# Optimization experiments

Hardware: AMD Instinct MI355X
Metric: run time of the kernel (lower is better)

## Reference

```python
import jax, jax.numpy as jnp
import numpy as np

K = 3
KK = K * K
EPS = 1e-5


def conv2d(x, w, b, pad):
    y = jax.lax.conv_general_dilated(x, w, (1, 1), [(pad, pad), (pad, pad)],
                                     dimension_numbers=("NCHW", "OIHW", "NCHW"))
    return y + b[None, :, None, None]


def bn(x, g, b, m, v):
    inv = g / jnp.sqrt(v + EPS)
    return x * inv[None, :, None, None] + (b - m * inv)[None, :, None, None]


def deform_sample(x, dy, dx):
    # x: [B,C,H,W]; dy,dx: [B,KK,H,W] -> sampled [B,C,KK,H,W] (bilinear, zeros outside)
    B, C, H, W = x.shape
    k = jnp.arange(K, dtype=x.dtype) - 1.0  # pad=1, dilation=1, stride=1
    ky = jnp.repeat(k, K)  # [KK] row offsets
    kx = jnp.tile(k, K)    # [KK] col offsets
    hh = jnp.arange(H, dtype=x.dtype)
    ww = jnp.arange(W, dtype=x.dtype)
    py = hh[None, :, None] + ky[:, None, None] + dy  # [B,KK,H,W]
    px = ww[None, None, :] + kx[:, None, None] + dx

    def sample_one(img, py, px):
        y0f = jnp.floor(py); x0f = jnp.floor(px)
        wy = py - y0f; wx = px - x0f
        y0 = y0f.astype(jnp.int32); x0 = x0f.astype(jnp.int32)

        def gather(yi, xi, w):
            valid = (yi >= 0) & (yi < H) & (xi >= 0) & (xi < W)
            yc = jnp.clip(yi, 0, H - 1); xc = jnp.clip(xi, 0, W - 1)
            v = img[:, yc, xc]  # [C,KK,H,W]
            return v * (w * valid)[None]

        return (gather(y0, x0, (1 - wy) * (1 - wx)) +
                gather(y0, x0 + 1, (1 - wy) * wx) +
                gather(y0 + 1, x0, wy * (1 - wx)) +
                gather(y0 + 1, x0 + 1, wy * wx))

    return jax.vmap(sample_one)(x, py, px)


def setup_inputs() -> dict:
    key = jax.random.key(0)
    ks = jax.random.split(key, 16)
    B, C, H, W = 8, 256, 64, 64
    d = {
        "feature": jax.random.normal(ks[0], (B, C, H, W), jnp.float32),
        "p1_w": jax.random.normal(ks[1], (C, C, 1, 1), jnp.float32) * 0.05,
        "p1_b": jax.random.normal(ks[2], (C,), jnp.float32) * 0.05,
        "bn1_g": jax.random.normal(ks[3], (C,), jnp.float32) * 0.1 + 1.0,
        "bn1_b": jax.random.normal(ks[4], (C,), jnp.float32) * 0.05,
        "bn1_m": jax.random.normal(ks[5], (C,), jnp.float32) * 0.05,
        "bn1_v": jax.random.uniform(ks[6], (C,), jnp.float32) + 0.5,
        "off_w": jax.random.normal(ks[7], (3 * KK, 2 * C, K, K), jnp.float32) * 0.01,
        "off_b": jax.random.normal(ks[8], (3 * KK,), jnp.float32) * 0.01,
        "dcn_w": jax.random.normal(ks[9], (C, C, K, K), jnp.float32) * 0.05,
        "dcn_b": jax.random.normal(ks[10], (C,), jnp.float32) * 0.05,
        "bn2_g": jax.random.normal(ks[11], (C,), jnp.float32) * 0.1 + 1.0,
        "bn2_b": jax.random.normal(ks[12], (C,), jnp.float32) * 0.05,
        "bn2_m": jax.random.normal(ks[13], (C,), jnp.float32) * 0.05,
        "bn2_v": jax.random.uniform(ks[14], (C,), jnp.float32) + 0.5,
    }
    return d


def reference(feature, p1_w, p1_b, bn1_g, bn1_b, bn1_m, bn1_v,
              off_w, off_b, dcn_w, dcn_b, bn2_g, bn2_b, bn2_m, bn2_v):
    flipped = feature[..., ::-1]                      # flip last (W) axis
    proj = bn(conv2d(feature, p1_w, p1_b, 0), bn1_g, bn1_b, bn1_m, bn1_v)
    # DCNv2: offsets/mask from concat(flipped, proj)
    concat = jnp.concatenate([flipped, proj], axis=1)
    off = conv2d(concat, off_w, off_b, 1)             # [B,27,H,W]
    dy = off[:, :KK]
    dx = off[:, KK:2 * KK]
    mask = jax.nn.sigmoid(off[:, 2 * KK:])            # [B,KK,H,W]
    sampled = deform_sample(flipped, dy, dx)          # [B,C,KK,H,W]
    O = dcn_w.shape[0]
    y = jnp.einsum("bckhw,ock->bohw", sampled * mask[:, None], dcn_w.reshape(O, -1, KK))
    y = y + dcn_b[None, :, None, None]
    y = bn(y, bn2_g, bn2_b, bn2_m, bn2_v)
    return jax.nn.relu(proj + y)
```

## Files before the change

kernel.cpp:

```cpp
#include <hip/hip_runtime.h>
#include <hip/hip_bf16.h>
#include <math.h>

typedef __attribute__((ext_vector_type(8))) short short8;
typedef __attribute__((ext_vector_type(4))) short short4v;
typedef __attribute__((ext_vector_type(4))) float f32x4;
typedef __attribute__((ext_vector_type(2))) float f32x2;

__device__ __forceinline__ float bs2f(short s){
    union { unsigned u; float f; } x; x.u = ((unsigned)(unsigned short)s) << 16; return x.f;
}
__device__ __forceinline__ short f2bs(float f){
    union { float f; unsigned u; } x; x.f = f;
    unsigned r = x.u + 0x7fff + ((x.u >> 16) & 1);
    return (short)(r >> 16);
}
__device__ __forceinline__ f32x2 up2(unsigned u){
    union { unsigned u; float f; } lo, hi;
    lo.u = u << 16; hi.u = u & 0xffff0000u;
    f32x2 r; r.x = lo.f; r.y = hi.f; return r;
}
__device__ __forceinline__ unsigned pk2rn(float lo, float hi){
    __hip_bfloat162 h = __float22bfloat162_rn(make_float2(lo, hi));
    union { __hip_bfloat162 h; unsigned u; } cv; cv.h = h; return cv.u;
}
__device__ __forceinline__ void gl2lds16(const void* g, void* l){
    __builtin_amdgcn_global_load_lds(
        (const __attribute__((address_space(1))) void*)g,
        (__attribute__((address_space(3))) void*)l, 16, 0, 0);
}
__device__ __forceinline__ void hard_barrier(){
    __builtin_amdgcn_sched_barrier(0);
    __builtin_amdgcn_s_barrier();
    __builtin_amdgcn_sched_barrier(0);
}

#define XPB ((size_t)66*66*512)


__global__ void k_prep(const float* __restrict__ p1_w, const float* __restrict__ p1_b,
                       const float* __restrict__ bn1_g, const float* __restrict__ bn1_b,
                       const float* __restrict__ bn1_m, const float* __restrict__ bn1_v,
                       const float* __restrict__ off_w,
                       const float* __restrict__ dcn_w, const float* __restrict__ dcn_b,
                       const float* __restrict__ bn2_g, const float* __restrict__ bn2_b,
                       const float* __restrict__ bn2_m, const float* __restrict__ bn2_v,
                       short* __restrict__ p1_wb, short* __restrict__ Woffb,
                       short* __restrict__ Wbf,
                       float* __restrict__ bias1f, float* __restrict__ inv2f,
                       float* __restrict__ bias2f, unsigned* __restrict__ XpadU)
{
    int blk = blockIdx.x, t = threadIdx.x;
    if (blk == 0) {
        float inv1 = bn1_g[t] / sqrtf(bn1_v[t] + 1e-5f);
        bias1f[t] = p1_b[t] * inv1 + bn1_b[t] - bn1_m[t] * inv1;
        float inv2 = bn2_g[t] / sqrtf(bn2_v[t] + 1e-5f);
        inv2f[t] = inv2;
        bias2f[t] = dcn_b[t] * inv2 + bn2_b[t] - bn2_m[t] * inv2;
    } else if (blk <= 256) {
        int o = blk - 1;
        float inv1 = bn1_g[o] / sqrtf(bn1_v[o] + 1e-5f);
        p1_wb[o*256 + t] = f2bs(p1_w[o*256 + t] * inv1);
    } else if (blk <= 512) {
        int o = blk - 257;
        const float* src = dcn_w + (size_t)o*2304;
        #pragma unroll
        for (int j = 0; j < 9; ++j)
            Wbf[(size_t)o*2304 + j*256 + t] = f2bs(src[t*9 + j]);
    } else if (blk <= 544) {
        int oc = blk - 513;
        if (oc < 27) {
            const float* src = off_w + (size_t)oc*4608;
            #pragma unroll
            for (int j = 0; j < 18; ++j) {
                int e = j*256 + t, tap = e >> 9, ci = e & 511;
                Woffb[(size_t)oc*4608 + e] = f2bs(src[ci*9 + tap]);
            }
        } else {
            #pragma unroll
            for (int j = 0; j < 18; ++j)
                Woffb[(size_t)oc*4608 + j*256 + t] = 0;
        }
    } else {
        int hb = blk - 545;
        int b = hb / 260, i = hb % 260;
        int y, x;
        if (i < 66)       { y = 0;  x = i; }
        else if (i < 132) { y = 65; x = i - 66; }
        else { int j = i - 132; y = 1 + (j >> 1); x = (j & 1) * 65; }
        XpadU[((size_t)(b*66 + y)*66 + x)*256 + t] = 0u;
    }
}

__global__ void k_featT(const float* __restrict__ feature, short* __restrict__ Xpad)
{
    __shared__ float tile[64][65];
    int bb = blockIdx.x;
    int b = bb & 7, h = (bb >> 3) & 63, cg = bb >> 9;
    int c0 = cg * 64;
    int t = threadIdx.x;
    int lw = t & 63, li = t >> 6;
    #pragma unroll
    for (int j = 0; j < 16; ++j) {
        int cl = j*4 + li;
        tile[cl][63 - lw] = feature[((b*256 + c0 + cl)*64 + h)*64 + lw];
    }
    __syncthreads();
    #pragma unroll
    for (int j = 0; j < 16; ++j) {
        int wl = j*4 + li;
        Xpad[((size_t)(b*66 + h+1)*66 + (wl+1))*512 + c0 + lw] = f2bs(tile[lw][wl]);
    }
}

__global__ __launch_bounds__(512, 4) void k_projm(
    short* Xpad, const short* __restrict__ p1_wb, const float* __restrict__ bias1f)
{
    __shared__ short Ash[256*32];
    __shared__ short Bsh[64*32];
    int bid = blockIdx.x;
    int b = bid & 7, h = bid >> 3;
    int t = threadIdx.x;
    int lane = t & 63, w = t >> 6;
    int ln = lane & 15, q = lane >> 4;
    int r16 = lane >> 2;
    int sq  = (lane & 3) ^ ((lane >> 3) & 3);
    int rq  = (q ^ ((ln >> 1) & 3)) * 8;
    size_t rowbase = (size_t)(b*66 + h + 1)*66;

    f32x4 acc[2][4] = {};
    for (int kt = 0; kt < 8; ++kt) {
        int kcol = kt*32 + sq*8;
        #pragma unroll
        for (int i = 0; i < 2; ++i) {
            int row = w*32 + i*16 + r16;
            gl2lds16(p1_wb + (size_t)row*256 + kcol, Ash + (w*32 + i*16)*32);
        }
        if (w < 4) {
            int x = w*16 + r16;
            gl2lds16(Xpad + (rowbase + (64 - x))*512 + kcol, Bsh + (w*16)*32);
        }
        __syncthreads();
        short8 af[2], bfr[4];
        #pragma unroll
        for (int i = 0; i < 2; ++i)
            af[i] = *(const short8*)&Ash[(w*32 + i*16 + ln)*32 + rq];
        #pragma unroll
        for (int j = 0; j < 4; ++j)
            bfr[j] = *(const short8*)&Bsh[(j*16 + ln)*32 + rq];
        #pragma unroll
        for (int i = 0; i < 2; ++i)
            #pragma unroll
            for (int j = 0; j < 4; ++j)
                acc[i][j] = __builtin_amdgcn_mfma_f32_16x16x32_bf16(af[i], bfr[j], acc[i][j], 0, 0, 0);
        __syncthreads();
    }
    #pragma unroll
    for (int i = 0; i < 2; ++i) {
        int ob = w*32 + i*16 + q*4;
        #pragma unroll
        for (int j = 0; j < 4; ++j) {
            int x = j*16 + ln;
            size_t xb = (rowbase + x + 1)*512 + 256 + ob;
            short4v st;
            st.x = f2bs(acc[i][j][0] + bias1f[ob]);
            st.y = f2bs(acc[i][j][1] + bias1f[ob+1]);
            st.z = f2bs(acc[i][j][2] + bias1f[ob+2]);
            st.w = f2bs(acc[i][j][3] + bias1f[ob+3]);
            *(short4v*)&Xpad[xb] = st;
        }
    }
}

__global__ __launch_bounds__(512, 4) void k_offm(
    const short* __restrict__ Xpad, const short* __restrict__ Woffb,
    const float* __restrict__ off_b, float* __restrict__ offv)
{
    __shared__ short Ash[8][32*32];
    __shared__ short Bsh[8][64*32];
    int bid = blockIdx.x;
    int b = bid & 7, h = bid >> 3;
    int t = threadIdx.x;
    int lane = t & 63, w = t >> 6;
    int ln = lane & 15, q = lane >> 4;
    int wr = w >> 2, wc = w & 3;
    int r16 = lane >> 2;
    int sq  = (lane & 3) ^ ((lane >> 3) & 3);
    int rq  = (q ^ ((ln >> 1) & 3)) * 8;
    const short* xb = Xpad + (size_t)b*XPB;

    f32x4 acc = {};
    for (int it = 0; it < 18; ++it) {
        #pragma unroll
        for (int s = 0; s < 8; ++s) {
            int k = it*256 + s*32;
            int tap = k >> 9;
            int dy = tap/3 - 1, dx = tap%3 - 1;
            if (w < 4) {
                int row = w*16 + r16;
                const short* gB = xb + ((size_t)(h + 1 + dy)*66 + (row + dx + 1))*512
                                     + (k & 511) + sq*8;
                gl2lds16(gB, &Bsh[s][(w*16)*32]);
            } else if (w < 6) {
                int row = (w-4)*16 + r16;
                const short* gA = Woffb + (size_t)row*4608 + k + sq*8;
                gl2lds16(gA, &Ash[s][((w-4)*16)*32]);
            }
        }
        __syncthreads();
        #pragma unroll
        for (int s = 0; s < 8; ++s) {
            short8 af  = *(const short8*)&Ash[s][(wr*16 + ln)*32 + rq];
            short8 bfr = *(const short8*)&Bsh[s][(wc*16 + ln)*32 + rq];
            acc = __builtin_amdgcn_mfma_f32_16x16x32_bf16(af, bfr, acc, 0, 0, 0);
        }
        __syncthreads();
    }
    int x = wc*16 + ln;
    #pragma unroll
    for (int r = 0; r < 4; ++r) {
        int oc = wr*16 + q*4 + r;
        if (oc < 27)
            offv[((b*27 + oc)*64 + h)*64 + x] = acc[r] + off_b[oc];
    }
}

__global__ __launch_bounds__(512, 4) void k_gemm(
    const short* __restrict__ Xpad,
    const short* __restrict__ Wbf,
    const float* __restrict__ offv,
    const float* __restrict__ inv2f, const float* __restrict__ bias2f,
    float* __restrict__ out)
{
    __shared__ __align__(16) short Ash[2][256*32];
    __shared__ __align__(16) short Bsh[2][64*32];
    __shared__ unsigned c_pk[576];
    __shared__ float c_w[576*4];
    int bid = blockIdx.x;
    int b = bid & 7, h = bid >> 3;
    int t = threadIdx.x;
    int lane = t & 63, w = t >> 6;
    int ln = lane & 15, q = lane >> 4;
    int r16 = lane >> 2;
    int sq  = (lane & 3) ^ ((lane >> 3) & 3);
    int rq  = (q ^ ((ln >> 1) & 3)) * 8;

    for (int e = t; e < 576; e += 512) {
        int p = e / 9, k = e % 9;
        int base = (b*27)*4096 + h*64 + p;
        float dy = offv[base + k*4096];
        float dx = offv[base + (9+k)*4096];
        float ms = offv[base + (18+k)*4096];
        ms = 1.f / (1.f + expf(-ms));
        float py = (float)h + (float)(k/3 - 1) + dy;
        float px = (float)p + (float)(k%3 - 1) + dx;
        float y0f = floorf(py), x0f = floorf(px);
        float wy = py - y0f, wx = px - x0f;
        int y0 = (int)y0f, x0 = (int)x0f;
        int y1 = y0 + 1, x1 = x0 + 1;
        float vy0 = (y0 >= 0 && y0 < 64) ? 1.f : 0.f;
        float vy1 = (y1 >= 0 && y1 < 64) ? 1.f : 0.f;
        float vx0 = (x0 >= 0 && x0 < 64) ? 1.f : 0.f;
        float vx1 = (x1 >= 0 && x1 < 64) ? 1.f : 0.f;
        int y0c = min(max(y0,0),63), y1c = min(max(y1,0),63);
        int x0c = min(max(x0,0),63), x1c = min(max(x1,0),63);
        unsigned cell = (unsigned)(((y0c+1)*66 + x0c+1)*128);
        unsigned sx = (x1c != x0c) ? 1u : 0u;
        unsigned sy = (y1c != y0c) ? 1u : 0u;
        c_pk[e] = cell | (sx << 20) | (sy << 21);
        c_w[e*4+0] = ms * (1.f-wy)*(1.f-wx) * vy0*vx0;
        c_w[e*4+1] = ms * (1.f-wy)*wx       * vy0*vx1;
        c_w[e*4+2] = ms * wy*(1.f-wx)       * vy1*vx0;
        c_w[e*4+3] = ms * wy*wx             * vy1*vx1;
    }
    __syncthreads();

    const uint2* fT = (const uint2*)Xpad + (size_t)b*(XPB/4);
    int pr = t >> 3;
    int jo = t & 7;
    int pe9 = pr*9;
    short* bdst = &Bsh[jo >> 2][pr*32 + (((jo & 3) ^ ((pr >> 1) & 3)) << 3)];

    f32x4 acc[2][4] = {};
    uint4 U[4], V[4];

    auto GATHER = [&](int win, uint4 (&dst)[4]) {
        unsigned pw = c_pk[pe9 + (win >> 2)];
        int o00 = pw & 0xFFFFF;
        int dxs = (pw >> 13) & 128;
        int dys = ((pw >> 8) & 0x2000) | ((pw >> 13) & 0x100);
        int cin = ((win & 3) << 4) + jo*2;
        const uint2* p0 = fT + (o00 + cin);
        dst[0] = *(const uint4*)(p0);
        dst[1] = *(const uint4*)(p0 + dxs);
        dst[2] = *(const uint4*)(p0 + dys);
        dst[3] = *(const uint4*)(p0 + dys + dxs);
    };

    auto WIN = [&](int kc2, uint4 (&uc)[4], uint4 (&vn)[4]) {
        int tap = kc2 >> 2;
        #pragma unroll
        for (int s = 0; s < 2; ++s) {
            int kcol = (kc2*2 + s)*32 + sq*8;
            #pragma unroll
            for (int i = 0; i < 2; ++i) {
                int row = w*32 + i*16 + r16;
                gl2lds16(Wbf + (size_t)row*2304 + kcol, &Ash[s][(w*32 + i*16)*32]);
            }
        }
        __builtin_amdgcn_sched_barrier(0);
        GATHER(kc2 < 35 ? kc2 + 1 : 35, vn);
        const float4 cw = *(const float4*)&c_w[(pe9 + tap)*4];
        f32x2 Wx; Wx.x = cw.x; Wx.y = cw.x;
        f32x2 Wy; Wy.x = cw.y; Wy.y = cw.y;
        f32x2 Wz; Wz.x = cw.z; Wz.y = cw.z;
        f32x2 Ww; Ww.x = cw.w; Ww.y = cw.w;
        f32x2 G0 = Wx*up2(uc[0].x) + Wy*up2(uc[1].x) + Wz*up2(uc[2].x) + Ww*up2(uc[3].x);
        f32x2 G1 = Wx*up2(uc[0].y) + Wy*up2(uc[1].y) + Wz*up2(uc[2].y) + Ww*up2(uc[3].y);
        f32x2 G2 = Wx*up2(uc[0].z) + Wy*up2(uc[1].z) + Wz*up2(uc[2].z) + Ww*up2(uc[3].z);
        f32x2 G3 = Wx*up2(uc[0].w) + Wy*up2(uc[1].w) + Wz*up2(uc[2].w) + Ww*up2(uc[3].w);
        uint4 pkv;
        pkv.x = pk2rn(G0.x, G0.y);
        pkv.y = pk2rn(G1.x, G1.y);
        pkv.z = pk2rn(G2.x, G2.y);
        pkv.w = pk2rn(G3.x, G3.y);
        *(uint4*)bdst = pkv;
        asm volatile("s_waitcnt vmcnt(4) lgkmcnt(0)" ::: "memory");
        hard_barrier();
        #pragma unroll
        for (int s = 0; s < 2; ++s) {
            short8 af[2], bfr[4];
            #pragma unroll
            for (int i = 0; i < 2; ++i)
                af[i] = *(const short8*)&Ash[s][(w*32 + i*16 + ln)*32 + rq];
            #pragma unroll
            for (int jj = 0; jj < 4; ++jj)
                bfr[jj] = *(const short8*)&Bsh[s][(jj*16 + ln)*32 + rq];
            #pragma unroll
            for (int i = 0; i < 2; ++i)
                #pragma unroll
                for (int jj = 0; jj < 4; ++jj)
                    acc[i][jj] = __builtin_amdgcn_mfma_f32_16x16x32_bf16(af[i], bfr[jj], acc[i][jj], 0, 0, 0);
        }
        hard_barrier();
    };

    GATHER(0, U);
    __builtin_amdgcn_sched_barrier(0);
    for (int kc2 = 0; kc2 < 36; kc2 += 2) {
        WIN(kc2, U, V);
        WIN(kc2 + 1, V, U);
    }

    #pragma unroll
    for (int i = 0; i < 2; ++i) {
        int ob = w*32 + i*16 + q*4;
        #pragma unroll
        for (int jj = 0; jj < 4; ++jj) {
            int p = jj*16 + ln;
            size_t xb = ((size_t)(b*66 + h + 1)*66 + p + 1)*512 + 256 + ob;
            short4v prr = *(const short4v*)&Xpad[xb];
            #pragma unroll
            for (int r = 0; r < 4; ++r) {
                int o = ob + r;
                size_t idx = ((size_t)(b*256 + o))*4096 + h*64 + p;
                float rs = bs2f(((const short*)&prr)[r]);
                float v = rs + acc[i][jj][r]*inv2f[o] + bias2f[o];
                out[idx] = v < 0.f ? 0.f : v;
            }
        }
    }
}

extern "C" void kernel_launch(void* const* d_in, const int* in_sizes, int n_in,
                              void* d_out, int out_size, void* d_ws, size_t ws_size,
                              hipStream_t stream)
{
    const float* feature = (const float*)d_in[0];
    const float* p1_w  = (const float*)d_in[1];
    const float* p1_b  = (const float*)d_in[2];
    const float* bn1_g = (const float*)d_in[3];
    const float* bn1_b = (const float*)d_in[4];
    const float* bn1_m = (const float*)d_in[5];
    const float* bn1_v = (const float*)d_in[6];
    const float* off_w = (const float*)d_in[7];
    const float* off_b = (const float*)d_in[8];
    const float* dcn_w = (const float*)d_in[9];
    const float* dcn_b = (const float*)d_in[10];
    const float* bn2_g = (const float*)d_in[11];
    const float* bn2_b = (const float*)d_in[12];
    const float* bn2_m = (const float*)d_in[13];
    const float* bn2_v = (const float*)d_in[14];

    float* ws = (float*)d_ws;
    short* Xpad   = (short*)ws;
    float* offbuf = ws + 8921088;
    short* p1_wb  = (short*)(ws + 9805824);
    short* Woffb  = (short*)(ws + 9838592);
    short* Wbf    = (short*)(ws + 9912320);
    float* bias1f = ws + 10207232;
    float* inv2f  = ws + 10207488;
    float* bias2f = ws + 10207744;

    k_prep<<<2625, 256, 0, stream>>>(p1_w, p1_b, bn1_g, bn1_b, bn1_m, bn1_v,
                                     off_w, dcn_w, dcn_b, bn2_g, bn2_b, bn2_m, bn2_v,
                                     p1_wb, Woffb, Wbf, bias1f, inv2f, bias2f,
                                     (unsigned*)Xpad);
    k_featT<<<2048, 256, 0, stream>>>(feature, Xpad);
    k_projm<<<512, 512, 0, stream>>>(Xpad, p1_wb, bias1f);
    k_offm<<<512, 512, 0, stream>>>(Xpad, Woffb, off_b, offbuf);
    k_gemm<<<512, 512, 0, stream>>>(Xpad, Wbf, offbuf, inv2f, bias2f, (float*)d_out);
}
```

Baseline: 218.9 us.

## Replace direct global-to-LDS loads with register-prefetched double buffering in GEMM kernels

Both the projection GEMM and the deformable-conv GEMM stop using global_load_lds for weight/activation tiles. They now load the next tile into registers one step ahead and write the current tile to LDS just before the barrier. The aim is to hide global load latency behind the MFMA work of the previous step, instead of waiting on vmcnt before each barrier. In exchange the kernels use more VGPRs, which can lower occupancy, and they spend extra instructions on the register-to-LDS store.

After: 392.5 us. +79.3%, slower.

```diff
diff --git a/kernel.cpp b/kernel.cpp
--- a/kernel.cpp
+++ b/kernel.cpp
@@ -31,6 +31,12 @@
 }
 __device__ __forceinline__ void hard_barrier(){
     __builtin_amdgcn_sched_barrier(0);
+    __builtin_amdgcn_s_barrier();
+    __builtin_amdgcn_sched_barrier(0);
+}
+__device__ __forceinline__ void lds_barrier(){
+    __builtin_amdgcn_sched_barrier(0);
+    asm volatile("s_waitcnt lgkmcnt(0)" ::: "memory");
     __builtin_amdgcn_s_barrier();
     __builtin_amdgcn_sched_barrier(0);
 }
@@ -116,8 +122,8 @@
 __global__ __launch_bounds__(512, 4) void k_projm(
     short* Xpad, const short* __restrict__ p1_wb, const float* __restrict__ bias1f)
 {
-    __shared__ short Ash[256*32];
-    __shared__ short Bsh[64*32];
+    __shared__ __align__(16) short Ash[256*32];
+    __shared__ __align__(16) short Bsh[64*32];
     int bid = blockIdx.x;
     int b = bid & 7, h = bid >> 3;
     int t = threadIdx.x;
@@ -129,18 +135,26 @@
     size_t rowbase = (size_t)(b*66 + h + 1)*66;
 
     f32x4 acc[2][4] = {};
-    for (int kt = 0; kt < 8; ++kt) {
+    uint4 a0[2], a1[2], b0, b1;
+
+    auto LOADR = [&](int kt, uint4 (&ar)[2], uint4& br){
         int kcol = kt*32 + sq*8;
         #pragma unroll
-        for (int i = 0; i < 2; ++i) {
-            int row = w*32 + i*16 + r16;
-            gl2lds16(p1_wb + (size_t)row*256 + kcol, Ash + (w*32 + i*16)*32);
-        }
+        for (int i = 0; i < 2; ++i)
+            ar[i] = *(const uint4*)(p1_wb + (size_t)(w*32 + i*16 + r16)*256 + kcol);
         if (w < 4) {
             int x = w*16 + r16;
-            gl2lds16(Xpad + (rowbase + (64 - x))*512 + kcol, Bsh + (w*16)*32);
-        }
-        __syncthreads();
+            br = *(const uint4*)(Xpad + (rowbase + (64 - x))*512 + kcol);
+        }
+    };
+    auto WRITE = [&](uint4 (&ar)[2], uint4& br){
+        #pragma unroll
+        for (int i = 0; i < 2; ++i)
+            *(uint4*)&Ash[(w*32 + i*16)*32 + lane*8] = ar[i];
+        if (w < 4)
+            *(uint4*)&Bsh[(w*16)*32 + lane*8] = br;
+    };
+    auto MM = [&](){
         short8 af[2], bfr[4];
         #pragma unroll
         for (int i = 0; i < 2; ++i)
@@ -153,7 +167,24 @@
             #pragma unroll
             for (int j = 0; j < 4; ++j)
                 acc[i][j] = __builtin_amdgcn_mfma_f32_16x16x32_bf16(af[i], bfr[j], acc[i][j], 0, 0, 0);
-        __syncthreads();
+    };
+
+    LOADR(0, a0, b0);
+    __builtin_amdgcn_sched_barrier(0);
+    #pragma unroll 1
+    for (int kt = 0; kt < 8; kt += 2) {
+        LOADR(kt + 1, a1, b1);
+        __builtin_amdgcn_sched_barrier(0);
+        WRITE(a0, b0);
+        lds_barrier();
+        MM();
+        hard_barrier();
+        LOADR(kt < 6 ? kt + 2 : 7, a0, b0);
+        __builtin_amdgcn_sched_barrier(0);
+        WRITE(a1, b1);
+        lds_barrier();
+        MM();
+        hard_barrier();
     }
     #pragma unroll
     for (int i = 0; i < 2; ++i) {
@@ -283,6 +314,7 @@
 
     f32x4 acc[2][4] = {};
     uint4 U[4], V[4];
+    uint4 A0[4], A1[4];
 
     auto GATHER = [&](int win, uint4 (&dst)[4]) {
         unsigned pw = c_pk[pe9 + (win >> 2)];
@@ -296,20 +328,22 @@
         dst[2] = *(const uint4*)(p0 + dys);
         dst[3] = *(const uint4*)(p0 + dys + dxs);
     };
-
-    auto WIN = [&](int kc2, uint4 (&uc)[4], uint4 (&vn)[4]) {
+    auto ALOADR = [&](int kc2, uint4 (&ar)[4]) {
+        #pragma unroll
+        for (int s = 0; s < 2; ++s)
+            #pragma unroll
+            for (int i = 0; i < 2; ++i)
+                ar[s*2+i] = *(const uint4*)(Wbf
+                    + (size_t)(w*32 + i*16 + r16)*2304 + (kc2*2 + s)*32 + sq*8);
+    };
+
+    auto WIN = [&](int kc2, uint4 (&arC)[4], uint4 (&arN)[4],
+                   uint4 (&uc)[4], uint4 (&vn)[4]) {
+        int kn = kc2 < 35 ? kc2 + 1 : 35;
+        ALOADR(kn, arN);
+        GATHER(kn, vn);
+        __builtin_amdgcn_sched_barrier(0);
         int tap = kc2 >> 2;
-        #pragma unroll
-        for (int s = 0; s < 2; ++s) {
-            int kcol = (kc2*2 + s)*32 + sq*8;
-            #pragma unroll
-            for (int i = 0; i < 2; ++i) {
-                int row = w*32 + i*16 + r16;
-                gl2lds16(Wbf + (size_t)row*2304 + kcol, &Ash[s][(w*32 + i*16)*32]);
-            }
-        }
-        __builtin_amdgcn_sched_barrier(0);
-        GATHER(kc2 < 35 ? kc2 + 1 : 35, vn);
         const float4 cw = *(const float4*)&c_w[(pe9 + tap)*4];
         f32x2 Wx; Wx.x = cw.x; Wx.y = cw.x;
         f32x2 Wy; Wy.x = cw.y; Wy.y = cw.y;
@@ -325,8 +359,12 @@
         pkv.z = pk2rn(G2.x, G2.y);
         pkv.w = pk2rn(G3.x, G3.y);
         *(uint4*)bdst = pkv;
-        asm volatile("s_waitcnt vmcnt(4) lgkmcnt(0)" ::: "memory");
-        hard_barrier();
+        #pragma unroll
+        for (int s = 0; s < 2; ++s)
+            #pragma unroll
+            for (int i = 0; i < 2; ++i)
+                *(uint4*)&Ash[s][(w*32 + i*16)*32 + lane*8] = arC[s*2+i];
+        lds_barrier();
         #pragma unroll
         for (int s = 0; s < 2; ++s) {
             short8 af[2], bfr[4];
@@ -345,11 +383,12 @@
         hard_barrier();
     };
 
+    ALOADR(0, A0);
     GATHER(0, U);
     __builtin_amdgcn_sched_barrier(0);
     for (int kc2 = 0; kc2 < 36; kc2 += 2) {
-        WIN(kc2, U, V);
-        WIN(kc2 + 1, V, U);
+        WIN(kc2,     A0, A1, U, V);
+        WIN(kc2 + 1, A1, A0, V, U);
     }
 
     #pragma unroll
```

## Load DCN weights directly into registers in MFMA fragment layout, drop LDS staging

Applied to the files above, without the earlier changes.

The prep kernel now writes the deformable-conv weights pre-swizzled into MFMA A-fragment order, so each lane reads its fragment straight from global memory into registers. The LDS A tile and its global-to-LDS copies go away. The A fragments for the next window are prefetched into registers alongside the gather, and the MFMA phase waits only on LDS. This removes LDS traffic and the vmcnt wait, at the cost of more VGPRs, so launch bounds drop from 4 to 3 waves per SIMD and occupancy may fall.

Measured after the change: 220.1 us. No clear change (+0.5%).

```diff
diff --git a/kernel.cpp b/kernel.cpp
--- a/kernel.cpp
+++ b/kernel.cpp
@@ -31,6 +31,12 @@
 }
 __device__ __forceinline__ void hard_barrier(){
     __builtin_amdgcn_sched_barrier(0);
+    __builtin_amdgcn_s_barrier();
+    __builtin_amdgcn_sched_barrier(0);
+}
+__device__ __forceinline__ void lds_barrier(){
+    __builtin_amdgcn_sched_barrier(0);
+    asm volatile("s_waitcnt lgkmcnt(0)" ::: "memory");
     __builtin_amdgcn_s_barrier();
     __builtin_amdgcn_sched_barrier(0);
 }
@@ -46,7 +52,7 @@
                        const float* __restrict__ bn2_g, const float* __restrict__ bn2_b,
                        const float* __restrict__ bn2_m, const float* __restrict__ bn2_v,
                        short* __restrict__ p1_wb, short* __restrict__ Woffb,
-                       short* __restrict__ Wbf,
+                       short* __restrict__ Wfrag,
                        float* __restrict__ bias1f, float* __restrict__ inv2f,
                        float* __restrict__ bias2f, unsigned* __restrict__ XpadU)
 {
@@ -64,9 +70,20 @@
     } else if (blk <= 512) {
         int o = blk - 257;
         const float* src = dcn_w + (size_t)o*2304;
-        #pragma unroll
-        for (int j = 0; j < 9; ++j)
-            Wbf[(size_t)o*2304 + j*256 + t] = f2bs(src[t*9 + j]);
+        uint4* dst = (uint4*)Wfrag;
+        int strip = o >> 4, lnn = o & 15;
+        #pragma unroll
+        for (int r = 0; r < 2; ++r) {
+            int j = r*256 + t;
+            if (j < 288) {
+                int tap = j >> 5, c0 = (j & 31) * 8;
+                union { short s[8]; uint4 u; } v;
+                #pragma unroll
+                for (int e = 0; e < 8; ++e)
+                    v.s[e] = f2bs(src[(c0 + e)*9 + tap]);
+                dst[(size_t)((j >> 2)*16 + strip)*64 + (j & 3)*16 + lnn] = v.u;
+            }
+        }
     } else if (blk <= 544) {
         int oc = blk - 513;
         if (oc < 27) {
@@ -225,14 +242,50 @@
     }
 }
 
-__global__ __launch_bounds__(512, 4) void k_gemm(
+#define ALOAD4(kn_, A_)                                                   \
+    A_##0 = Wf4[(size_t)(((kn_)*2+0)*16 + tw0)*64 + lane];                \
+    A_##1 = Wf4[(size_t)(((kn_)*2+0)*16 + tw1)*64 + lane];                \
+    A_##2 = Wf4[(size_t)(((kn_)*2+1)*16 + tw0)*64 + lane];                \
+    A_##3 = Wf4[(size_t)(((kn_)*2+1)*16 + tw1)*64 + lane];
+
+#define MMPHASE(A_)                                                       \
+    {                                                                     \
+        short8 af00 = *(short8*)&A_##0, af01 = *(short8*)&A_##1;          \
+        short8 af10 = *(short8*)&A_##2, af11 = *(short8*)&A_##3;          \
+        short8 bfr;                                                       \
+        _Pragma("unroll")                                                 \
+        for (int jj = 0; jj < 4; ++jj) {                                  \
+            bfr = *(const short8*)&Bsh[0][(jj*16 + ln)*32 + rq];          \
+            acc[0][jj] = __builtin_amdgcn_mfma_f32_16x16x32_bf16(af00, bfr, acc[0][jj], 0, 0, 0); \
+            acc[1][jj] = __builtin_amdgcn_mfma_f32_16x16x32_bf16(af01, bfr, acc[1][jj], 0, 0, 0); \
+        }                                                                 \
+        _Pragma("unroll")                                                 \
+        for (int jj = 0; jj < 4; ++jj) {                                  \
+            bfr = *(const short8*)&Bsh[1][(jj*16 + ln)*32 + rq];          \
+            acc[0][jj] = __builtin_amdgcn_mfma_f32_16x16x32_bf16(af10, bfr, acc[0][jj], 0, 0, 0); \
+            acc[1][jj] = __builtin_amdgcn_mfma_f32_16x16x32_bf16(af11, bfr, acc[1][jj], 0, 0, 0); \
+        }                                                                 \
+    }
+
+#define WINX(kc2_, AC_, AN_, UC_, VN_)                                    \
+    {                                                                     \
+        int kn_ = (kc2_) < 35 ? (kc2_) + 1 : 35;                          \
+        ALOAD4(kn_, AN_);                                                 \
+        GATHER(kn_, VN_);                                                 \
+        __builtin_amdgcn_sched_barrier(0);                                \
+        BLEND(UC_, (kc2_) >> 2);                                          \
+        lds_barrier();                                                    \
+        MMPHASE(AC_);                                                     \
+        hard_barrier();                                                   \
+    }
+
+__global__ __launch_bounds__(512, 3) void k_gemm(
     const short* __restrict__ Xpad,
-    const short* __restrict__ Wbf,
+    const short* __restrict__ Wfrag,
     const float* __restrict__ offv,
     const float* __restrict__ inv2f, const float* __restrict__ bias2f,
     float* __restrict__ out)
 {
-    __shared__ __align__(16) short Ash[2][256*32];
     __shared__ __align__(16) short Bsh[2][64*32];
     __shared__ unsigned c_pk[576];
     __shared__ float c_w[576*4];
@@ -241,9 +294,9 @@
     int t = threadIdx.x;
     int lane = t & 63, w = t >> 6;
     int ln = lane & 15, q = lane >> 4;
-    int r16 = lane >> 2;
-    int sq  = (lane & 3) ^ ((lane >> 3) & 3);
     int rq  = (q ^ ((ln >> 1) & 3)) * 8;
+    int tw0 = w*2, tw1 = w*2 + 1;
+    const uint4* Wf4 = (const uint4*)Wfrag;
 
     for (int e = t; e < 576; e += 512) {
         int p = e / 9, k = e % 9;
@@ -283,6 +336,8 @@
 
     f32x4 acc[2][4] = {};
     uint4 U[4], V[4];
+    uint4 a00, a01, a02, a03;
+    uint4 a10, a11, a12, a13;
 
     auto GATHER = [&](int win, uint4 (&dst)[4]) {
         unsigned pw = c_pk[pe9 + (win >> 2)];
@@ -296,20 +351,7 @@
         dst[2] = *(const uint4*)(p0 + dys);
         dst[3] = *(const uint4*)(p0 + dys + dxs);
     };
-
-    auto WIN = [&](int kc2, uint4 (&uc)[4], uint4 (&vn)[4]) {
-        int tap = kc2 >> 2;
-        #pragma unroll
-        for (int s = 0; s < 2; ++s) {
-            int kcol = (kc2*2 + s)*32 + sq*8;
-            #pragma unroll
-            for (int i = 0; i < 2; ++i) {
-                int row = w*32 + i*16 + r16;
-                gl2lds16(Wbf + (size_t)row*2304 + kcol, &Ash[s][(w*32 + i*16)*32]);
-            }
-        }
-        __builtin_amdgcn_sched_barrier(0);
-        GATHER(kc2 < 35 ? kc2 + 1 : 35, vn);
+    auto BLEND = [&](uint4 (&uc)[4], int tap) {
         const float4 cw = *(const float4*)&c_w[(pe9 + tap)*4];
         f32x2 Wx; Wx.x = cw.x; Wx.y = cw.x;
         f32x2 Wy; Wy.x = cw.y; Wy.y = cw.y;
@@ -325,31 +367,15 @@
         pkv.z = pk2rn(G2.x, G2.y);
         pkv.w = pk2rn(G3.x, G3.y);
         *(uint4*)bdst = pkv;
-        asm volatile("s_waitcnt vmcnt(4) lgkmcnt(0)" ::: "memory");
-        hard_barrier();
-        #pragma unroll
-        for (int s = 0; s < 2; ++s) {
-            short8 af[2], bfr[4];
-            #pragma unroll
-            for (int i = 0; i < 2; ++i)
-                af[i] = *(const short8*)&Ash[s][(w*32 + i*16 + ln)*32 + rq];
-            #pragma unroll
-            for (int jj = 0; jj < 4; ++jj)
-                bfr[jj] = *(const short8*)&Bsh[s][(jj*16 + ln)*32 + rq];
-            #pragma unroll
-            for (int i = 0; i < 2; ++i)
-                #pragma unroll
-                for (int jj = 0; jj < 4; ++jj)
-                    acc[i][jj] = __builtin_amdgcn_mfma_f32_16x16x32_bf16(af[i], bfr[jj], acc[i][jj], 0, 0, 0);
-        }
-        hard_barrier();
     };
 
+    ALOAD4(0, a0);
     GATHER(0, U);
     __builtin_amdgcn_sched_barrier(0);
+    #pragma unroll 1
     for (int kc2 = 0; kc2 < 36; kc2 += 2) {
-        WIN(kc2, U, V);
-        WIN(kc2 + 1, V, U);
+        WINX(kc2,     a0, a1, U, V);
+        WINX(kc2 + 1, a1, a0, V, U);
     }
 
     #pragma unroll
@@ -397,17 +423,17 @@
     float* offbuf = ws + 8921088;
     short* p1_wb  = (short*)(ws + 9805824);
     short* Woffb  = (short*)(ws + 9838592);
-    short* Wbf    = (short*)(ws + 9912320);
+    short* Wfrag  = (short*)(ws + 9912320);
     float* bias1f = ws + 10207232;
     float* inv2f  = ws + 10207488;
     float* bias2f = ws + 10207744;
 
     k_prep<<<2625, 256, 0, stream>>>(p1_w, p1_b, bn1_g, bn1_b, bn1_m, bn1_v,
                                      off_w, dcn_w, dcn_b, bn2_g, bn2_b, bn2_m, bn2_v,
-                                     p1_wb, Woffb, Wbf, bias1f, inv2f, bias2f,
+                                     p1_wb, Woffb, Wfrag, bias1f, inv2f, bias2f,
                                      (unsigned*)Xpad);
     k_featT<<<2048, 256, 0, stream>>>(feature, Xpad);
     k_projm<<<512, 512, 0, stream>>>(Xpad, p1_wb, bias1f);
     k_offm<<<512, 512, 0, stream>>>(Xpad, Woffb, off_b, offbuf);
-    k_gemm<<<512, 512, 0, stream>>>(Xpad, Wbf, offbuf, inv2f, bias2f, (float*)d_out);
-}
+    k_gemm<<<512, 512, 0, stream>>>(Xpad, Wfrag, offbuf, inv2f, bias2f, (float*)d_out);
+}
```
